# Optimization experiments

Hardware: AMD Instinct MI355X
Metric: run time of the kernel (lower is better)

The kernel has to match this reference:

```python
import jax, jax.numpy as jnp
import numpy as np

B, S, D = 2, 2048, 640
H, DH = 8, 80  # heads, dim_head
SCALE = DH ** -0.5


def setup_inputs() -> dict:
    key = jax.random.key(0)
    ks = jax.random.split(key, 7)
    std = D ** -0.5
    return {
        "x": jax.random.normal(ks[0], (B, S, D), jnp.float32),
        "encoder_hidden_states": jax.random.normal(ks[1], (B, S, D), jnp.float32),
        # Linear weights stored as [in, out] so application is x @ W
        "Wq": jax.random.normal(ks[2], (D, H * DH), jnp.float32) * std,
        "Wk": jax.random.normal(ks[3], (D, H * DH), jnp.float32) * std,
        "Wv": jax.random.normal(ks[4], (D, H * DH), jnp.float32) * std,
        "Wo": jax.random.normal(ks[5], (H * DH, D), jnp.float32) * std,
        "bo": jax.random.normal(ks[6], (D,), jnp.float32) * 0.01,
    }


def reference(x, encoder_hidden_states, Wq, Wk, Wv, Wo, bo):
    # projections (to_q/to_k/to_v have bias=False)
    q = x @ Wq                      # [B, S, H*DH]
    k = encoder_hidden_states @ Wk  # [B, S, H*DH]
    v = encoder_hidden_states @ Wv  # [B, S, H*DH]

    def split_heads(t):
        b, s, _ = t.shape
        return t.reshape(b, s, H, DH).transpose(0, 2, 1, 3)  # [B, H, S, DH]

    q, k, v = split_heads(q), split_heads(k), split_heads(v)

    # the torch loop over bh-chunks computes plain softmax attention; same math fused
    scores = jnp.einsum("bhid,bhjd->bhij", q, k) * SCALE  # [B, H, Sq, Skv]
    attn = jax.nn.softmax(scores, axis=-1)
    out = jnp.einsum("bhij,bhjd->bhid", attn, v)          # [B, H, Sq, DH]

    out = out.transpose(0, 2, 1, 3).reshape(x.shape[0], x.shape[1], H * DH)
    return out @ Wo + bo  # to_out[0]; Dropout(p=0) is identity
```

## Files before the change

kernel.cpp:

```cpp
#include <hip/hip_runtime.h>
#include <hip/hip_bf16.h>

typedef __bf16 v4bf __attribute__((ext_vector_type(4)));
typedef __bf16 v8bf __attribute__((ext_vector_type(8)));
typedef float  v4f  __attribute__((ext_vector_type(4)));

namespace {
constexpr int Bb  = 2;
constexpr int Ss  = 2048;
constexpr int Dd  = 640;
constexpr int Hh  = 8;
constexpr int DHh = 80;
constexpr int Mm  = Bb * Ss;
constexpr float kQScale = 0.11180339887498949f * 1.4426950408889634f;

__device__ __forceinline__ float4 ld4(const float* p) {
  return *reinterpret_cast<const float4*>(p);
}

__device__ __forceinline__ v8bf pack8(float4 f0, float4 f1) {
  v8bf p;
  p[0]=(__bf16)f0.x; p[1]=(__bf16)f0.y; p[2]=(__bf16)f0.z; p[3]=(__bf16)f0.w;
  p[4]=(__bf16)f1.x; p[5]=(__bf16)f1.y; p[6]=(__bf16)f1.z; p[7]=(__bf16)f1.w;
  return p;
}

__device__ __forceinline__ float exp2_hw(float x) {
  float r;
  asm("v_exp_f32 %0, %1" : "=v"(r) : "v"(x));
  return r;
}
}

__global__ __launch_bounds__(256)
void wtrans_kernel(const float* __restrict__ Wq, const float* __restrict__ Wk,
                   const float* __restrict__ Wv, const float* __restrict__ Wo,
                   __bf16* __restrict__ Wtq, __bf16* __restrict__ Wtk,
                   __bf16* __restrict__ Wtv, __bf16* __restrict__ Wto) {
  const int z = blockIdx.z;
  const float* W = (z == 0) ? Wq : (z == 1) ? Wk : (z == 2) ? Wv : Wo;
  __bf16* Wt = (z == 0) ? Wtq : (z == 1) ? Wtk : (z == 2) ? Wtv : Wto;
  const int k0 = blockIdx.y * 32, n0 = blockIdx.x * 32;
  __shared__ float t[32][33];
  const int tid = threadIdx.x;
  {
    int kr = tid >> 3, c4 = (tid & 7) * 4;
    float4 f = ld4(W + (size_t)(k0 + kr) * Dd + n0 + c4);
    t[kr][c4 + 0] = f.x; t[kr][c4 + 1] = f.y;
    t[kr][c4 + 2] = f.z; t[kr][c4 + 3] = f.w;
  }
  __syncthreads();
  {
    int nr = tid >> 3, kc = (tid & 7) * 4;
    v4bf p;
#pragma unroll
    for (int u = 0; u < 4; ++u) p[u] = (__bf16)t[kc + u][nr];
    *reinterpret_cast<v4bf*>(&Wt[(size_t)(n0 + nr) * Dd + k0 + kc]) = p;
  }
}

__device__ __forceinline__ void gemm_core_db(const float* __restrict__ Af,
                                             const __bf16* __restrict__ Bt,
                                             __bf16* As, __bf16* Bs, int m0,
                                             int n0, int rh, int ch,
                                             v4f acc[4][4]) {
  constexpr int BUF = 128 * 40;
  constexpr int NKB = Dd / 32;
  const int tid = threadIdx.x;
  const int lane = tid & 63;
  const int quad = lane >> 4, l15 = lane & 15;
  const int lr = tid >> 1;
  const int lk = (tid & 1) * 16;
  const __bf16* Bg = Bt + (size_t)(n0 + lr) * Dd + lk;

#pragma unroll
  for (int i = 0; i < 4; ++i)
#pragma unroll
    for (int j = 0; j < 4; ++j) acc[i][j] = (v4f){0.f, 0.f, 0.f, 0.f};

  v8bf a0, a1, b0, b1;
  {
    const float* ap = Af + (size_t)(m0 + lr) * Dd + lk;
    a0 = pack8(ld4(ap), ld4(ap + 4));
    a1 = pack8(ld4(ap + 8), ld4(ap + 12));
  }
  b0 = *reinterpret_cast<const v8bf*>(Bg);
  b1 = *reinterpret_cast<const v8bf*>(Bg + 8);
  *reinterpret_cast<v8bf*>(&As[lr * 40 + lk])     = a0;
  *reinterpret_cast<v8bf*>(&As[lr * 40 + lk + 8]) = a1;
  *reinterpret_cast<v8bf*>(&Bs[lr * 40 + lk])     = b0;
  *reinterpret_cast<v8bf*>(&Bs[lr * 40 + lk + 8]) = b1;

  for (int it = 0; it < NKB; ++it) {
    if (it + 1 < NKB) {
      const int kb = (it + 1) * 32;
      const float* ap = Af + (size_t)(m0 + lr) * Dd + kb + lk;
      a0 = pack8(ld4(ap), ld4(ap + 4));
      a1 = pack8(ld4(ap + 8), ld4(ap + 12));
      b0 = *reinterpret_cast<const v8bf*>(Bg + kb);
      b1 = *reinterpret_cast<const v8bf*>(Bg + kb + 8);
    }
    __syncthreads();
    const int cur = (it & 1) * BUF, nxt = BUF - cur;
    v8bf af[4], bv[4];
#pragma unroll
    for (int i = 0; i < 4; ++i)
      af[i] = *reinterpret_cast<const v8bf*>(
          &As[cur + (rh + i * 16 + l15) * 40 + quad * 8]);
#pragma unroll
    for (int j = 0; j < 4; ++j)
      bv[j] = *reinterpret_cast<const v8bf*>(
          &Bs[cur + (ch + j * 16 + l15) * 40 + quad * 8]);
#pragma unroll
    for (int i = 0; i < 4; ++i)
#pragma unroll
      for (int j = 0; j < 4; ++j)
        acc[i][j] = __builtin_amdgcn_mfma_f32_16x16x32_bf16(af[i], bv[j],
                                                            acc[i][j], 0, 0, 0);
    if (it + 1 < NKB) {
      *reinterpret_cast<v8bf*>(&As[nxt + lr * 40 + lk])     = a0;
      *reinterpret_cast<v8bf*>(&As[nxt + lr * 40 + lk + 8]) = a1;
      *reinterpret_cast<v8bf*>(&Bs[nxt + lr * 40 + lk])     = b0;
      *reinterpret_cast<v8bf*>(&Bs[nxt + lr * 40 + lk + 8]) = b1;
    }
  }
}

__global__ __launch_bounds__(256)
void gemm_qkv_mfma(const float* __restrict__ x, const float* __restrict__ ehs,
                   const __bf16* __restrict__ Wtq,
                   const __bf16* __restrict__ Wtk,
                   const __bf16* __restrict__ Wtv, __bf16* __restrict__ qb,
                   __bf16* __restrict__ kbuf, __bf16* __restrict__ vb) {
  const int z = blockIdx.z;
  const float* A = (z == 0) ? x : ehs;
  const __bf16* Bt = (z == 0) ? Wtq : (z == 1) ? Wtk : Wtv;
  __bf16* C = (z == 0) ? qb : (z == 1) ? kbuf : vb;
  const float scale = (z == 0) ? kQScale : 1.0f;

  __shared__ __bf16 As[2 * 128 * 40];
  __shared__ __bf16 Bs[2 * 128 * 40];
  const int tid = threadIdx.x;
  const int w = tid >> 6, lane = tid & 63;
  const int quad = lane >> 4, l15 = lane & 15;
  const int m0 = blockIdx.y * 128, n0 = blockIdx.x * 128;
  const int rh = (w >> 1) * 64, ch = (w & 1) * 64;
  v4f acc[4][4];
  gemm_core_db(A, Bt, As, Bs, m0, n0, rh, ch, acc);

  if (z == 2) {
#pragma unroll
    for (int i = 0; i < 4; ++i)
#pragma unroll
      for (int j = 0; j < 4; ++j) {
        int m = m0 + rh + i * 16 + quad * 4;
        int n = n0 + ch + j * 16 + l15;
        int hh = n / DHh, d = n % DHh;
        int bb = m >> 11, tok = m & 2047;
        int tb = tok >> 5, t = tok & 31;
        v4bf pk;
#pragma unroll
        for (int r = 0; r < 4; ++r) pk[r] = (__bf16)acc[i][j][r];
        *reinterpret_cast<v4bf*>(
            &C[((((size_t)bb * Hh + hh) * (Ss / 32) + tb) * DHh + d) * 32 +
               t]) = pk;
      }
  } else {
#pragma unroll
    for (int i = 0; i < 4; ++i)
#pragma unroll
      for (int j = 0; j < 4; ++j) {
        int m = m0 + rh + i * 16 + quad * 4;
        int n = n0 + ch + j * 16 + l15;
        int hh = n / DHh, d = n % DHh;
        int bb = m >> 11, tok = m & 2047;
        __bf16* base = &C[(((size_t)bb * Hh + hh) * Ss + tok) * DHh + d];
#pragma unroll
        for (int r = 0; r < 4; ++r)
          base[(size_t)r * DHh] = (__bf16)(acc[i][j][r] * scale);
      }
  }
}

__global__ __launch_bounds__(256)
void gemm_out_mfma(const __bf16* __restrict__ A, const __bf16* __restrict__ Bt,
                   const float* __restrict__ bias, float* __restrict__ out) {
  constexpr int BUFA = 128 * 40, BUFB = 64 * 40;
  constexpr int NKB = Dd / 32;
  __shared__ __bf16 As[2 * BUFA];
  __shared__ __bf16 Bs[2 * BUFB];
  const int tid = threadIdx.x;
  const int w = tid >> 6, lane = tid & 63;
  const int quad = lane >> 4, l15 = lane & 15;
  const int m0 = blockIdx.y * 128, n0 = blockIdx.x * 64;
  const int rh = (w >> 1) * 64, ch = (w & 1) * 32;
  const int lrA = tid >> 1, lkA = (tid & 1) * 16;
  const int lrB = tid >> 2, lkB = (tid & 3) * 8;
  const __bf16* Ag = A + (size_t)(m0 + lrA) * Dd + lkA;
  const __bf16* Bg = Bt + (size_t)(n0 + lrB) * Dd + lkB;

  v4f acc[4][2];
#pragma unroll
  for (int i = 0; i < 4; ++i)
#pragma unroll
    for (int j = 0; j < 2; ++j) acc[i][j] = (v4f){0.f, 0.f, 0.f, 0.f};

  v8bf a0, a1, b0;
  a0 = *reinterpret_cast<const v8bf*>(Ag);
  a1 = *reinterpret_cast<const v8bf*>(Ag + 8);
  b0 = *reinterpret_cast<const v8bf*>(Bg);
  *reinterpret_cast<v8bf*>(&As[lrA * 40 + lkA])     = a0;
  *reinterpret_cast<v8bf*>(&As[lrA * 40 + lkA + 8]) = a1;
  *reinterpret_cast<v8bf*>(&Bs[lrB * 40 + lkB])     = b0;

  for (int it = 0; it < NKB; ++it) {
    if (it + 1 < NKB) {
      const int kb = (it + 1) * 32;
      a0 = *reinterpret_cast<const v8bf*>(Ag + kb);
      a1 = *reinterpret_cast<const v8bf*>(Ag + kb + 8);
      b0 = *reinterpret_cast<const v8bf*>(Bg + kb);
    }
    __syncthreads();
    const int curA = (it & 1) * BUFA, nxtA = BUFA - curA;
    const int curB = (it & 1) * BUFB, nxtB = BUFB - curB;
    v8bf af[4], bv[2];
#pragma unroll
    for (int i = 0; i < 4; ++i)
      af[i] = *reinterpret_cast<const v8bf*>(
          &As[curA + (rh + i * 16 + l15) * 40 + quad * 8]);
#pragma unroll
    for (int j = 0; j < 2; ++j)
      bv[j] = *reinterpret_cast<const v8bf*>(
          &Bs[curB + (ch + j * 16 + l15) * 40 + quad * 8]);
#pragma unroll
    for (int i = 0; i < 4; ++i)
#pragma unroll
      for (int j = 0; j < 2; ++j)
        acc[i][j] = __builtin_amdgcn_mfma_f32_16x16x32_bf16(af[i], bv[j],
                                                            acc[i][j], 0, 0, 0);
    if (it + 1 < NKB) {
      *reinterpret_cast<v8bf*>(&As[nxtA + lrA * 40 + lkA])     = a0;
      *reinterpret_cast<v8bf*>(&As[nxtA + lrA * 40 + lkA + 8]) = a1;
      *reinterpret_cast<v8bf*>(&Bs[nxtB + lrB * 40 + lkB])     = b0;
    }
  }

#pragma unroll
  for (int i = 0; i < 4; ++i)
#pragma unroll
    for (int j = 0; j < 2; ++j) {
      int m = m0 + rh + i * 16 + quad * 4;
      int n = n0 + ch + j * 16 + l15;
      float bn = bias[n];
#pragma unroll
      for (int r = 0; r < 4; ++r)
        out[(size_t)(m + r) * Dd + n] = acc[i][j][r] + bn;
    }
}

__global__ __launch_bounds__(256, 2)
void attn_mfma_kernel(const __bf16* __restrict__ q,
                      const __bf16* __restrict__ k,
                      const __bf16* __restrict__ vtg, __bf16* __restrict__ o) {
  constexpr int QT = 64;
  constexpr int KT = 32;
  constexpr int KW = Ss / 4;
  constexpr int NIT = KW / KT;
  constexpr int LQ = 104;
  constexpr int LV = 40;
  constexpr int KS = KT * LQ;
  constexpr int VS = 96 * LV;
  constexpr int PS = QT * LV;
  constexpr int WSZ = KS + VS + PS;
  constexpr int LM = 100;

  __shared__ __align__(16) __bf16 smem[4 * WSZ];

  const int bh = blockIdx.x;
  const int b = bh >> 3, h = bh & 7;
  const int q0 = blockIdx.y * QT;
  const int tid = threadIdx.x;
  const int w = tid >> 6;
  const int lane = tid & 63;
  const int quad = lane >> 4;
  const int l15 = lane & 15;

  __bf16* ksw = smem + w * WSZ;
  __bf16* vtw = ksw + KS;
  __bf16* psw = vtw + VS;

  const __bf16* qg  = q + ((size_t)(b * Hh + h) * Ss + q0) * DHh;
  const __bf16* kgb = k + (size_t)(b * Hh + h) * Ss * DHh;
  const __bf16* vgb = vtg + (size_t)(b * Hh + h) * Ss * DHh;

  v8bf qf[4][3];
#pragma unroll
  for (int qt = 0; qt < 4; ++qt)
#pragma unroll
    for (int s = 0; s < 3; ++s) {
      if (s == 2 && quad >= 2) {
        qf[qt][s] = (v8bf){};
      } else {
        qf[qt][s] = *reinterpret_cast<const v8bf*>(
            qg + (size_t)(qt * 16 + l15) * DHh + s * 32 + quad * 8);
      }
    }

  int klr[5];
#pragma unroll
  for (int c = 0; c < 5; ++c) {
    int E = c * 512 + lane * 8;
    klr[c] = (E / DHh) * LQ + (E % DHh);
  }
  const int vlo = (lane >> 2) * LV + (lane & 3) * 8;

  {
    v8bf z8 = {};
    *reinterpret_cast<v8bf*>(&ksw[(lane >> 1) * LQ + 80 + (lane & 1) * 8]) = z8;
    v8bf pad = {};
    int vr = 80 + (lane >> 2);
    if (vr == 80) {
#pragma unroll
      for (int e = 0; e < 8; ++e) pad[e] = (__bf16)1.f;
    }
    *reinterpret_cast<v8bf*>(&vtw[vr * LV + (lane & 3) * 8]) = pad;
  }
  {
    const __bf16* kg = kgb + (size_t)(w * KW) * DHh;
#pragma unroll
    for (int c = 0; c < 5; ++c)
      *reinterpret_cast<v8bf*>(&ksw[klr[c]]) =
          *reinterpret_cast<const v8bf*>(kg + c * 512 + lane * 8);
  }

  v4f Oacc[4][6];
#pragma unroll
  for (int qt = 0; qt < 4; ++qt)
#pragma unroll
    for (int mt = 0; mt < 6; ++mt) Oacc[qt][mt] = (v4f){0.f, 0.f, 0.f, 0.f};

  for (int it = 0; it < NIT; ++it) {
    const bool pfK = (it + 1 < NIT);
    v8bf kreg[5];
    if (pfK) {
      const __bf16* kg = kgb + (size_t)(w * KW + (it + 1) * KT) * DHh;
#pragma unroll
      for (int c = 0; c < 5; ++c)
        kreg[c] = *reinterpret_cast<const v8bf*>(kg + c * 512 + lane * 8);
    }

    v4f sacc[4][2];
#pragma unroll
    for (int qt = 0; qt < 4; ++qt) {
      sacc[qt][0] = (v4f){0.f, 0.f, 0.f, 0.f};
      sacc[qt][1] = (v4f){0.f, 0.f, 0.f, 0.f};
    }
    __builtin_amdgcn_s_setprio(1);
#pragma unroll
    for (int s = 0; s < 3; ++s) {
      v8bf ak0 = *reinterpret_cast<const v8bf*>(
          &ksw[l15 * LQ + s * 32 + quad * 8]);
      v8bf ak1 = *reinterpret_cast<const v8bf*>(
          &ksw[(16 + l15) * LQ + s * 32 + quad * 8]);
#pragma unroll
      for (int qt = 0; qt < 4; ++qt) {
        sacc[qt][0] = __builtin_amdgcn_mfma_f32_16x16x32_bf16(
            ak0, qf[qt][s], sacc[qt][0], 0, 0, 0);
        sacc[qt][1] = __builtin_amdgcn_mfma_f32_16x16x32_bf16(
            ak1, qf[qt][s], sacc[qt][1], 0, 0, 0);
      }
    }

    v8bf vreg[5];
    {
      const __bf16* vg = vgb + (size_t)(w * 16 + it) * (KT * DHh);
#pragma unroll
      for (int c = 0; c < 5; ++c)
        vreg[c] = *reinterpret_cast<const v8bf*>(vg + c * 512 + lane * 8);
    }

    if (it > 0) {
      v8bf bp[4];
#pragma unroll
      for (int qt = 0; qt < 4; ++qt)
        bp[qt] = *reinterpret_cast<const v8bf*>(
            &psw[(qt * 16 + l15) * LV + quad * 8]);
#pragma unroll
      for (int mt = 0; mt < 6; ++mt) {
        v8bf av = *reinterpret_cast<const v8bf*>(
            &vtw[(mt * 16 + l15) * LV + quad * 8]);
#pragma unroll
        for (int qt = 0; qt < 4; ++qt)
          Oacc[qt][mt] = __builtin_amdgcn_mfma_f32_16x16x32_bf16(
              av, bp[qt], Oacc[qt][mt], 0, 0, 0);
      }
    }
    __builtin_amdgcn_s_setprio(0);

#pragma unroll
    for (int qt = 0; qt < 4; ++qt)
#pragma unroll
      for (int mt = 0; mt < 2; ++mt) {
        v4bf pk;
#pragma unroll
        for (int r = 0; r < 4; ++r)
          pk[r] = (__bf16)exp2_hw(sacc[qt][mt][r]);
        *reinterpret_cast<v4bf*>(
            &psw[(qt * 16 + l15) * LV + mt * 16 + quad * 4]) = pk;
      }

    if (pfK) {
#pragma unroll
      for (int c = 0; c < 5; ++c)
        *reinterpret_cast<v8bf*>(&ksw[klr[c]]) = kreg[c];
    }
#pragma unroll
    for (int c = 0; c < 5; ++c)
      *reinterpret_cast<v8bf*>(&vtw[vlo + c * 16 * LV]) = vreg[c];
  }

  {
    v8bf bp[4];
#pragma unroll
    for (int qt = 0; qt < 4; ++qt)
      bp[qt] = *reinterpret_cast<const v8bf*>(
          &psw[(qt * 16 + l15) * LV + quad * 8]);
    __builtin_amdgcn_s_setprio(1);
#pragma unroll
    for (int mt = 0; mt < 6; ++mt) {
      v8bf av = *reinterpret_cast<const v8bf*>(
          &vtw[(mt * 16 + l15) * LV + quad * 8]);
#pragma unroll
      for (int qt = 0; qt < 4; ++qt)
        Oacc[qt][mt] = __builtin_amdgcn_mfma_f32_16x16x32_bf16(
            av, bp[qt], Oacc[qt][mt], 0, 0, 0);
    }
    __builtin_amdgcn_s_setprio(0);
  }

  __syncthreads();
  float* mrg = (float*)smem;
  if (w >= 2) {
    float* base = mrg + (w - 2) * (QT * LM);
#pragma unroll
    for (int qt = 0; qt < 4; ++qt)
#pragma unroll
      for (int mt = 0; mt < 6; ++mt)
        *reinterpret_cast<v4f*>(
            &base[(qt * 16 + l15) * LM + mt * 16 + quad * 4]) = Oacc[qt][mt];
  }
  __syncthreads();
  if (w < 2) {
    const float* base = mrg + w * (QT * LM);
#pragma unroll
    for (int qt = 0; qt < 4; ++qt)
#pragma unroll
      for (int mt = 0; mt < 6; ++mt)
        Oacc[qt][mt] += *reinterpret_cast<const v4f*>(
            &base[(qt * 16 + l15) * LM + mt * 16 + quad * 4]);
  }
  __syncthreads();
  if (w == 1) {
#pragma unroll
    for (int qt = 0; qt < 4; ++qt)
#pragma unroll
      for (int mt = 0; mt < 6; ++mt)
        *reinterpret_cast<v4f*>(
            &mrg[(qt * 16 + l15) * LM + mt * 16 + quad * 4]) = Oacc[qt][mt];
  }
  __syncthreads();
  if (w == 0) {
#pragma unroll
    for (int qt = 0; qt < 4; ++qt)
#pragma unroll
      for (int mt = 0; mt < 6; ++mt)
        Oacc[qt][mt] += *reinterpret_cast<const v4f*>(
            &mrg[(qt * 16 + l15) * LM + mt * 16 + quad * 4]);
#pragma unroll
    for (int qt = 0; qt < 4; ++qt) {
      float lsum = __shfl(Oacc[qt][5][0], l15);
      float inv = 1.f / lsum;
      __bf16* og =
          o + (size_t)(b * Ss + q0 + qt * 16 + l15) * Dd + h * DHh;
#pragma unroll
      for (int mt = 0; mt < 5; ++mt) {
        v4bf pk;
#pragma unroll
        for (int r = 0; r < 4; ++r) pk[r] = (__bf16)(Oacc[qt][mt][r] * inv);
        *reinterpret_cast<v4bf*>(&og[mt * 16 + quad * 4]) = pk;
      }
    }
  }
}

extern "C" void kernel_launch(void* const* d_in, const int* in_sizes, int n_in,
                              void* d_out, int out_size, void* d_ws,
                              size_t ws_size, hipStream_t stream) {
  const float* x   = (const float*)d_in[0];
  const float* ehs = (const float*)d_in[1];
  const float* Wq  = (const float*)d_in[2];
  const float* Wk  = (const float*)d_in[3];
  const float* Wv  = (const float*)d_in[4];
  const float* Wo  = (const float*)d_in[5];
  const float* bo  = (const float*)d_in[6];
  float* out = (float*)d_out;

  __bf16* qb  = (__bf16*)d_ws;
  __bf16* kb  = qb + (size_t)Mm * Dd;
  __bf16* vb  = kb + (size_t)Mm * Dd;
  __bf16* ab  = vb + (size_t)Mm * Dd;
  __bf16* Wtq = ab + (size_t)Mm * Dd;
  __bf16* Wtk = Wtq + (size_t)Dd * Dd;
  __bf16* Wtv = Wtk + (size_t)Dd * Dd;
  __bf16* Wto = Wtv + (size_t)Dd * Dd;

  wtrans_kernel<<<dim3(Dd / 32, Dd / 32, 4), 256, 0, stream>>>(
      Wq, Wk, Wv, Wo, Wtq, Wtk, Wtv, Wto);
  gemm_qkv_mfma<<<dim3(Dd / 128, Mm / 128, 3), 256, 0, stream>>>(
      x, ehs, Wtq, Wtk, Wtv, qb, kb, vb);
  attn_mfma_kernel<<<dim3(Bb * Hh, Ss / 64), 256, 0, stream>>>(qb, kb, vb, ab);
  gemm_out_mfma<<<dim3(Dd / 64, Mm / 128), 256, 0, stream>>>(ab, Wto, bo,
                                                             out);
}
```

Measured before the change: 147.8 us.

## Load K and V MFMA fragments directly from global into registers, bypassing LDS

The attention kernel no longer stages K and transposed V tiles through per-wave shared memory. Each lane now loads its MFMA operand fragments straight from global memory into registers, prefetching the next K tile one iteration ahead. The ones-row used for the row-sum is built as a constant register fragment instead of a padded LDS row. This removes LDS writes and reads and shrinks shared memory to the merge buffer, which may raise occupancy, but the global loads are strided per lane, less coalesced, and need more registers.

```diff
diff --git a/kernel.cpp b/kernel.cpp
--- a/kernel.cpp
+++ b/kernel.cpp
@@ -266,15 +266,11 @@
   constexpr int KT = 32;
   constexpr int KW = Ss / 4;
   constexpr int NIT = KW / KT;
-  constexpr int LQ = 104;
   constexpr int LV = 40;
-  constexpr int KS = KT * LQ;
-  constexpr int VS = 96 * LV;
   constexpr int PS = QT * LV;
-  constexpr int WSZ = KS + VS + PS;
   constexpr int LM = 100;
 
-  __shared__ __align__(16) __bf16 smem[4 * WSZ];
+  __shared__ __align__(16) float smem_f[2 * QT * LM];
 
   const int bh = blockIdx.x;
   const int b = bh >> 3, h = bh & 7;
@@ -285,9 +281,7 @@
   const int quad = lane >> 4;
   const int l15 = lane & 15;
 
-  __bf16* ksw = smem + w * WSZ;
-  __bf16* vtw = ksw + KS;
-  __bf16* psw = vtw + VS;
+  __bf16* psw = reinterpret_cast<__bf16*>(smem_f) + w * PS;
 
   const __bf16* qg  = q + ((size_t)(b * Hh + h) * Ss + q0) * DHh;
   const __bf16* kgb = k + (size_t)(b * Hh + h) * Ss * DHh;
@@ -306,32 +300,23 @@
       }
     }
 
-  int klr[5];
-#pragma unroll
-  for (int c = 0; c < 5; ++c) {
-    int E = c * 512 + lane * 8;
-    klr[c] = (E / DHh) * LQ + (E % DHh);
-  }
-  const int vlo = (lane >> 2) * LV + (lane & 3) * 8;
-
-  {
-    v8bf z8 = {};
-    *reinterpret_cast<v8bf*>(&ksw[(lane >> 1) * LQ + 80 + (lane & 1) * 8]) = z8;
-    v8bf pad = {};
-    int vr = 80 + (lane >> 2);
-    if (vr == 80) {
-#pragma unroll
-      for (int e = 0; e < 8; ++e) pad[e] = (__bf16)1.f;
-    }
-    *reinterpret_cast<v8bf*>(&vtw[vr * LV + (lane & 3) * 8]) = pad;
-  }
-  {
-    const __bf16* kg = kgb + (size_t)(w * KW) * DHh;
-#pragma unroll
-    for (int c = 0; c < 5; ++c)
-      *reinterpret_cast<v8bf*>(&ksw[klr[c]]) =
-          *reinterpret_cast<const v8bf*>(kg + c * 512 + lane * 8);
-  }
+  v8bf av5 = {};
+  if (l15 == 0) {
+#pragma unroll
+    for (int e = 0; e < 8; ++e) av5[e] = (__bf16)1.f;
+  }
+
+  v8bf kc[3][2];
+#pragma unroll
+  for (int s = 0; s < 3; ++s)
+#pragma unroll
+    for (int h16 = 0; h16 < 2; ++h16) {
+      v8bf t = {};
+      if (!(s == 2 && quad >= 2))
+        t = *reinterpret_cast<const v8bf*>(
+            kgb + (size_t)(w * KW + h16 * 16 + l15) * DHh + s * 32 + quad * 8);
+      kc[s][h16] = t;
+    }
 
   v4f Oacc[4][6];
 #pragma unroll
@@ -339,14 +324,14 @@
 #pragma unroll
     for (int mt = 0; mt < 6; ++mt) Oacc[qt][mt] = (v4f){0.f, 0.f, 0.f, 0.f};
 
+  v8bf vf[5];
   for (int it = 0; it < NIT; ++it) {
-    const bool pfK = (it + 1 < NIT);
-    v8bf kreg[5];
-    if (pfK) {
-      const __bf16* kg = kgb + (size_t)(w * KW + (it + 1) * KT) * DHh;
-#pragma unroll
-      for (int c = 0; c < 5; ++c)
-        kreg[c] = *reinterpret_cast<const v8bf*>(kg + c * 512 + lane * 8);
+    if (it > 0) {
+      const __bf16* vg = vgb + (size_t)(w * 16 + (it - 1)) * (KT * DHh);
+#pragma unroll
+      for (int mt = 0; mt < 5; ++mt)
+        vf[mt] = *reinterpret_cast<const v8bf*>(vg + (mt * 16 + l15) * 32 +
+                                                quad * 8);
     }
 
     v4f sacc[4][2];
@@ -358,25 +343,28 @@
     __builtin_amdgcn_s_setprio(1);
 #pragma unroll
     for (int s = 0; s < 3; ++s) {
-      v8bf ak0 = *reinterpret_cast<const v8bf*>(
-          &ksw[l15 * LQ + s * 32 + quad * 8]);
-      v8bf ak1 = *reinterpret_cast<const v8bf*>(
-          &ksw[(16 + l15) * LQ + s * 32 + quad * 8]);
 #pragma unroll
       for (int qt = 0; qt < 4; ++qt) {
         sacc[qt][0] = __builtin_amdgcn_mfma_f32_16x16x32_bf16(
-            ak0, qf[qt][s], sacc[qt][0], 0, 0, 0);
+            kc[s][0], qf[qt][s], sacc[qt][0], 0, 0, 0);
         sacc[qt][1] = __builtin_amdgcn_mfma_f32_16x16x32_bf16(
-            ak1, qf[qt][s], sacc[qt][1], 0, 0, 0);
+            kc[s][1], qf[qt][s], sacc[qt][1], 0, 0, 0);
       }
     }
 
-    v8bf vreg[5];
-    {
-      const __bf16* vg = vgb + (size_t)(w * 16 + it) * (KT * DHh);
-#pragma unroll
-      for (int c = 0; c < 5; ++c)
-        vreg[c] = *reinterpret_cast<const v8bf*>(vg + c * 512 + lane * 8);
+    v8bf kn[3][2];
+    if (it + 1 < NIT) {
+#pragma unroll
+      for (int s = 0; s < 3; ++s)
+#pragma unroll
+        for (int h16 = 0; h16 < 2; ++h16) {
+          v8bf t = {};
+          if (!(s == 2 && quad >= 2))
+            t = *reinterpret_cast<const v8bf*>(
+                kgb + (size_t)(w * KW + (it + 1) * KT + h16 * 16 + l15) * DHh +
+                s * 32 + quad * 8);
+          kn[s][h16] = t;
+        }
     }
 
     if (it > 0) {
@@ -386,14 +374,15 @@
         bp[qt] = *reinterpret_cast<const v8bf*>(
             &psw[(qt * 16 + l15) * LV + quad * 8]);
 #pragma unroll
-      for (int mt = 0; mt < 6; ++mt) {
-        v8bf av = *reinterpret_cast<const v8bf*>(
-            &vtw[(mt * 16 + l15) * LV + quad * 8]);
+      for (int mt = 0; mt < 5; ++mt)
 #pragma unroll
         for (int qt = 0; qt < 4; ++qt)
           Oacc[qt][mt] = __builtin_amdgcn_mfma_f32_16x16x32_bf16(
-              av, bp[qt], Oacc[qt][mt], 0, 0, 0);
-      }
+              vf[mt], bp[qt], Oacc[qt][mt], 0, 0, 0);
+#pragma unroll
+      for (int qt = 0; qt < 4; ++qt)
+        Oacc[qt][5] = __builtin_amdgcn_mfma_f32_16x16x32_bf16(
+            av5, bp[qt], Oacc[qt][5], 0, 0, 0);
     }
     __builtin_amdgcn_s_setprio(0);
 
@@ -409,17 +398,20 @@
             &psw[(qt * 16 + l15) * LV + mt * 16 + quad * 4]) = pk;
       }
 
-    if (pfK) {
-#pragma unroll
-      for (int c = 0; c < 5; ++c)
-        *reinterpret_cast<v8bf*>(&ksw[klr[c]]) = kreg[c];
-    }
-#pragma unroll
-    for (int c = 0; c < 5; ++c)
-      *reinterpret_cast<v8bf*>(&vtw[vlo + c * 16 * LV]) = vreg[c];
+    if (it + 1 < NIT) {
+#pragma unroll
+      for (int s = 0; s < 3; ++s)
+#pragma unroll
+        for (int h16 = 0; h16 < 2; ++h16) kc[s][h16] = kn[s][h16];
+    }
   }
 
   {
+    const __bf16* vg = vgb + (size_t)(w * 16 + (NIT - 1)) * (KT * DHh);
+#pragma unroll
+    for (int mt = 0; mt < 5; ++mt)
+      vf[mt] = *reinterpret_cast<const v8bf*>(vg + (mt * 16 + l15) * 32 +
+                                              quad * 8);
     v8bf bp[4];
 #pragma unroll
     for (int qt = 0; qt < 4; ++qt)
@@ -427,19 +419,20 @@
           &psw[(qt * 16 + l15) * LV + quad * 8]);
     __builtin_amdgcn_s_setprio(1);
 #pragma unroll
-    for (int mt = 0; mt < 6; ++mt) {
-      v8bf av = *reinterpret_cast<const v8bf*>(
-          &vtw[(mt * 16 + l15) * LV + quad * 8]);
+    for (int mt = 0; mt < 5; ++mt)
 #pragma unroll
       for (int qt = 0; qt < 4; ++qt)
         Oacc[qt][mt] = __builtin_amdgcn_mfma_f32_16x16x32_bf16(
-            av, bp[qt], Oacc[qt][mt], 0, 0, 0);
-    }
+            vf[mt], bp[qt], Oacc[qt][mt], 0, 0, 0);
+#pragma unroll
+    for (int qt = 0; qt < 4; ++qt)
+      Oacc[qt][5] = __builtin_amdgcn_mfma_f32_16x16x32_bf16(
+          av5, bp[qt], Oacc[qt][5], 0, 0, 0);
     __builtin_amdgcn_s_setprio(0);
   }
 
   __syncthreads();
-  float* mrg = (float*)smem;
+  float* mrg = smem_f;
   if (w >= 2) {
     float* base = mrg + (w - 2) * (QT * LM);
 #pragma unroll
```

Measured after the change: 146.5 us. No clear change (-0.8%).
